# Performance work log

Hardware: AMD Instinct MI355X
Metric: run time of the kernel (lower is better)

The kernel has to match this reference:

```python
import jax, jax.numpy as jnp
import numpy as np

NUM_HEADS = 16


def setup_inputs() -> dict:
    key = jax.random.key(0)
    ks = jax.random.split(key, 7)
    B, S, H = 4, 1024, 1024
    s = 0.02
    return {
        "x": jax.random.normal(ks[0], (B, S, H), dtype=jnp.float32),
        "Wq": jax.random.normal(ks[1], (H, H), dtype=jnp.float32) * s,
        "bq": jax.random.normal(ks[2], (H,), dtype=jnp.float32) * s,
        "Wk": jax.random.normal(ks[3], (H, H), dtype=jnp.float32) * s,
        "bk": jax.random.normal(ks[4], (H,), dtype=jnp.float32) * s,
        "Wv": jax.random.normal(ks[5], (H, H), dtype=jnp.float32) * s,
        "bv": jax.random.normal(ks[6], (H,), dtype=jnp.float32) * s,
    }


def _split_heads(y, num_heads):
    # rearrange 'b s (h c) -> h b s c'
    b, s, hid = y.shape
    c = hid // num_heads
    return y.reshape(b, s, num_heads, c).transpose(2, 0, 1, 3)


def reference(x, Wq, bq, Wk, bk, Wv, bv):
    h = NUM_HEADS
    head_size = x.shape[-1] // h
    # torch Linear: y = x @ W.T + b
    q = _split_heads(x @ Wq.T + bq, h)  # [h,b,s,c]
    k = _split_heads(x @ Wk.T + bk, h)
    v = _split_heads(x @ Wv.T + bv, h)
    scores = jnp.einsum('hbfc,hbtc->hbft', q, k) / jnp.sqrt(
        jnp.asarray(head_size, x.dtype))
    patterns = jax.nn.softmax(scores, axis=-1)  # softmax over t
    # NOTE: faithful to source, contracts over f (query axis) per
    # einsum('hbft,hbfc->hbtc', patterns, value)
    av = jnp.einsum('hbft,hbfc->hbtc', patterns, v)  # [h,b,t,c]
    # rearrange 'h b s c -> b s (c h)'  (channel-major interleave)
    out = av.transpose(1, 2, 3, 0)  # [b,s,c,h]
    b, s, c, hh = out.shape
    return out.reshape(b, s, c * hh)
```

## Files before the change

kernel.cpp:

```cpp
#include <hip/hip_runtime.h>
#include <hip/hip_bf16.h>

typedef short bf16x8 __attribute__((ext_vector_type(8)));
typedef short bf16x4 __attribute__((ext_vector_type(4)));
typedef float f32x4 __attribute__((ext_vector_type(4)));
typedef unsigned short u16;

#define MFMA32(a, b, c) __builtin_amdgcn_mfma_f32_16x16x32_bf16(a, b, c, 0, 0, 0)

#if defined(__has_builtin)
#if __has_builtin(__builtin_amdgcn_mfma_f32_16x16x16bf16_1k)
#define HAVE_MFMA16 1
#define MFMA16(a, b, c) __builtin_amdgcn_mfma_f32_16x16x16bf16_1k(a, b, c, 0, 0, 0)
#endif
#endif
#ifndef HAVE_MFMA16
static __device__ inline f32x4 mfma16_asm(bf16x4 a, bf16x4 b, f32x4 c) {
    f32x4 d;
    asm volatile("v_mfma_f32_16x16x16_bf16 %0, %1, %2, %3\n\ts_nop 7\n\ts_nop 7"
                 : "=v"(d) : "v"(a), "v"(b), "v"(c));
    return d;
}
#define MFMA16(a, b, c) mfma16_asm(a, b, c)
#endif

__device__ inline float fexp2(float x) {
#if defined(__has_builtin) && __has_builtin(__builtin_amdgcn_exp2f)
    return __builtin_amdgcn_exp2f(x);
#else
    return exp2f(x);
#endif
}

__device__ inline u16 f2bf(float f) {
    unsigned u = __float_as_uint(f);
    unsigned r = (u + 0x7fffu + ((u >> 16) & 1u)) >> 16;
    return (u16)r;
}

__device__ inline float bf2f(u16 v) {
    return __uint_as_float(((unsigned)v) << 16);
}

__device__ inline void gload_lds16(const void* g, void* l) {
    __builtin_amdgcn_global_load_lds(
        (const __attribute__((address_space(1))) void*)g,
        (__attribute__((address_space(3))) void*)l, 16, 0, 0);
}

#define BARRIER() __builtin_amdgcn_s_barrier()

__device__ inline int swz(int row, int colbyte) {
    return row * 128 + (colbyte ^ ((row & 7) << 4));
}

__device__ inline void stage8k_512(const u16* __restrict__ g, int gstride,
                                   u16* lds, int tid) {
    int o = tid * 16;
    int row = o >> 7;
    int colb = (o & 127) ^ ((row & 7) << 4);
    gload_lds16(g + row * gstride + (colb >> 1), (char*)lds + o);
}

__device__ inline void stage16k_256(const u16* __restrict__ g, int gstride,
                                    u16* lds, int tid) {
#pragma unroll
    for (int j = 0; j < 4; j++) {
        int o = (tid + j * 256) * 16;
        int row = o >> 7;
        int colb = (o & 127) ^ ((row & 7) << 4);
        gload_lds16(g + row * gstride + (colb >> 1), (char*)lds + o);
    }
}

__global__ void k_convert(const float* __restrict__ src, u16* __restrict__ dst, int n) {
    int i = (blockIdx.x * blockDim.x + threadIdx.x) * 4;
    if (i < n) {
        float4 v = *reinterpret_cast<const float4*>(src + i);
        ushort4 o;
        o.x = f2bf(v.x); o.y = f2bf(v.y); o.z = f2bf(v.z); o.w = f2bf(v.w);
        *reinterpret_cast<ushort4*>(dst + i) = o;
    }
}

__global__ void k_convert3(const float* __restrict__ s0, const float* __restrict__ s1,
                           const float* __restrict__ s2, u16* __restrict__ dst) {
    const float* s = (blockIdx.y == 0) ? s0 : ((blockIdx.y == 1) ? s1 : s2);
    int i = (blockIdx.x * blockDim.x + threadIdx.x) * 4;
    float4 v = *reinterpret_cast<const float4*>(s + i);
    ushort4 o;
    o.x = f2bf(v.x); o.y = f2bf(v.y); o.z = f2bf(v.z); o.w = f2bf(v.w);
    *reinterpret_cast<ushort4*>(dst + blockIdx.y * 1048576 + i) = o;
}

__global__ __launch_bounds__(256, 3) void k_proj(
    const u16* __restrict__ xb, const u16* __restrict__ wb,
    const float* __restrict__ bq, const float* __restrict__ bk, const float* __restrict__ bv,
    u16* __restrict__ outQ, u16* __restrict__ outK, u16* __restrict__ outVt)
{
    __shared__ __align__(16) u16 As[8192];
    __shared__ __align__(16) u16 Bs[8192];
    const int tid = threadIdx.x;
    const int lane = tid & 63;
    const int w = tid >> 6;
    const int bid = blockIdx.x;
    const int xcd = bid & 7, idx = bid >> 3;
    const int mg = xcd & 3, ng = xcd >> 2;
    const int m0 = (mg * 8 + (idx & 7)) * 128;
    const int nfull = ng * 12 + (idx >> 3);
    const int widx = nfull >> 3;
    const int n0 = (nfull & 7) * 128;
    const u16* W = wb + widx * 1024 * 1024;
    const float* bias = (widx == 0) ? bq : ((widx == 1) ? bk : bv);

    const int wm = (w >> 1) * 64, wn = (w & 1) * 64;
    const int lm = lane & 15, lg = lane >> 4;

    f32x4 zero = {0.f, 0.f, 0.f, 0.f};
    f32x4 acc[4][4];
#pragma unroll
    for (int m = 0; m < 4; m++)
#pragma unroll
        for (int n = 0; n < 4; n++) acc[m][n] = zero;

    for (int it = 0; it < 16; ++it) {
        stage16k_256(xb + m0 * 1024 + it * 64, 1024, As, tid);
        stage16k_256(W + n0 * 1024 + it * 64, 1024, Bs, tid);
        __syncthreads();
        const char* Ab = (const char*)As;
        const char* Bb = (const char*)Bs;
#pragma unroll
        for (int kk = 0; kk < 2; kk++) {
            bf16x8 a[4], b[4];
#pragma unroll
            for (int m = 0; m < 4; m++)
                a[m] = *(const bf16x8*)(Ab + swz(wm + m * 16 + lm, kk * 64 + lg * 16));
#pragma unroll
            for (int n = 0; n < 4; n++)
                b[n] = *(const bf16x8*)(Bb + swz(wn + n * 16 + lm, kk * 64 + lg * 16));
#pragma unroll
            for (int m = 0; m < 4; m++)
#pragma unroll
                for (int n = 0; n < 4; n++)
                    acc[m][n] = MFMA32(a[m], b[n], acc[m][n]);
        }
        __syncthreads();
    }

#pragma unroll
    for (int n = 0; n < 4; n++) {
        int col = n0 + wn + n * 16 + lm;
        float bz = bias[col];
        int h = col >> 6, c = col & 63;
#pragma unroll
        for (int m = 0; m < 4; m++) {
#pragma unroll
            for (int r = 0; r < 4; r++) {
                int row = m0 + wm + m * 16 + lg * 4 + r;
                float v = acc[m][n][r] + bz;
                int bb = row >> 10, s = row & 1023;
                int hb = h * 4 + bb;
                if (widx == 0) {
                    outQ[(hb * 1024 + s) * 64 + c] = f2bf(v * 0.18033688011112042f);
                } else if (widx == 1) {
                    outK[(hb * 1024 + s) * 64 + c] = f2bf(v);
                } else {
                    outVt[(hb * 64 + c) * 1024 + s] = f2bf(v);
                }
            }
        }
    }
}

__global__ __launch_bounds__(512, 2) void k_stats(
    const u16* __restrict__ Q, const u16* __restrict__ K, u16* __restrict__ Vt)
{
    __shared__ __align__(16) u16 sK[2][4096];
    __shared__ float linv_lds[256];
    const int bid = blockIdx.x;
    const int hb = (bid & 7) * 8 + ((bid >> 3) & 7);
    const int fb = (bid >> 6) * 256;
    const int tid = threadIdx.x, lane = tid & 63, w = tid >> 6;
    const int lm = lane & 15, lg = lane >> 4;
    const u16* Qh = Q + hb * 65536;
    const u16* Kh = K + hb * 65536;
    u16* Vh = Vt + hb * 65536;

    bf16x8 a[2][2];
#pragma unroll
    for (int fg = 0; fg < 2; fg++) {
        const u16* qp = &Qh[(fb + w * 32 + fg * 16 + lm) * 64 + lg * 8];
        a[fg][0] = *(const bf16x8*)qp;
        a[fg][1] = *(const bf16x8*)(qp + 32);
    }

    float lrun[2][4] = {{0.f, 0.f, 0.f, 0.f}, {0.f, 0.f, 0.f, 0.f}};

    stage8k_512(Kh, 64, sK[0], tid);
    int cur = 0;
    for (int it = 0; it < 16; ++it) {
        if (it < 15) {
            stage8k_512(Kh + (it + 1) * 64 * 64, 64, sK[cur ^ 1], tid);
            asm volatile("s_waitcnt vmcnt(1)" ::: "memory");
        } else {
            asm volatile("s_waitcnt vmcnt(0)" ::: "memory");
        }
        BARRIER();
        const char* base = (const char*)sK[cur];
#pragma unroll
        for (int n = 0; n < 4; n++) {
            int r = n * 16 + lm;
            bf16x8 b0 = *(const bf16x8*)(base + swz(r, lg * 16));
            bf16x8 b1 = *(const bf16x8*)(base + swz(r, 64 + lg * 16));
#pragma unroll
            for (int fg = 0; fg < 2; fg++) {
                f32x4 z = {0.f, 0.f, 0.f, 0.f};
                z = MFMA32(a[fg][0], b0, z);
                z = MFMA32(a[fg][1], b1, z);
                lrun[fg][0] += fexp2(z[0]);
                lrun[fg][1] += fexp2(z[1]);
                lrun[fg][2] += fexp2(z[2]);
                lrun[fg][3] += fexp2(z[3]);
            }
        }
        BARRIER();
        cur ^= 1;
    }
#pragma unroll
    for (int fg = 0; fg < 2; fg++) {
#pragma unroll
        for (int r = 0; r < 4; r++) {
            float s = lrun[fg][r];
            s += __shfl_xor(s, 1);
            s += __shfl_xor(s, 2);
            s += __shfl_xor(s, 4);
            s += __shfl_xor(s, 8);
            if (lm == 0) linv_lds[w * 32 + fg * 16 + lg * 4 + r] = 1.0f / s;
        }
    }
    __syncthreads();
    {
        int c = tid >> 3, f8 = tid & 7;
#pragma unroll
        for (int j = 0; j < 4; j++) {
            int fl = f8 * 8 + j * 64;
            u16* vp = &Vh[c * 1024 + fb + fl];
            union { bf16x8 v; u16 e[8]; } uu, oo;
            uu.v = *(const bf16x8*)vp;
#pragma unroll
            for (int i = 0; i < 8; i++)
                oo.e[i] = f2bf(bf2f(uu.e[i]) * linv_lds[fl + i]);
            *(bf16x8*)vp = oo.v;
        }
    }
}

__global__ __launch_bounds__(512, 2) void k_av(
    const u16* __restrict__ Q, const u16* __restrict__ K, const u16* __restrict__ Vt,
    float* __restrict__ out)
{
    __shared__ __align__(16) u16 sQ[2][4096];
    __shared__ __align__(16) u16 sV[2][4096];
    const int bid = blockIdx.x;
    const int hb = (bid & 7) * 8 + ((bid >> 3) & 7);
    const int tb = (bid >> 6) * 256;
    const int tid = threadIdx.x, lane = tid & 63, w = tid >> 6;
    const int lm = lane & 15, lg = lane >> 4;
    const u16* Qh = Q + hb * 65536;
    const u16* Kh = K + hb * 65536;
    const u16* Vh = Vt + hb * 65536;

    bf16x8 bK[2][2];
#pragma unroll
    for (int tg = 0; tg < 2; tg++) {
        const u16* kp = &Kh[(tb + w * 32 + tg * 16 + lm) * 64 + lg * 8];
        bK[tg][0] = *(const bf16x8*)kp;
        bK[tg][1] = *(const bf16x8*)(kp + 32);
    }

    f32x4 zero = {0.f, 0.f, 0.f, 0.f};
    f32x4 accv[2][4];
#pragma unroll
    for (int tg = 0; tg < 2; tg++)
#pragma unroll
        for (int m = 0; m < 4; m++) accv[tg][m] = zero;

    stage8k_512(Qh, 64, sQ[0], tid);
    stage8k_512(Vh, 1024, sV[0], tid);

    int cur = 0;
    for (int it = 0; it < 16; ++it) {
        if (it < 15) {
            int fn = (it + 1) * 64;
            stage8k_512(Qh + fn * 64, 64, sQ[cur ^ 1], tid);
            stage8k_512(Vh + fn, 1024, sV[cur ^ 1], tid);
            asm volatile("s_waitcnt vmcnt(2)" ::: "memory");
        } else {
            asm volatile("s_waitcnt vmcnt(0)" ::: "memory");
        }
        BARRIER();
        const char* Qb = (const char*)sQ[cur];
        const char* Vb = (const char*)sV[cur];

        bf16x4 bv[4][4];
#pragma unroll
        for (int m = 0; m < 4; m++)
#pragma unroll
            for (int kc = 0; kc < 4; kc++)
                bv[m][kc] = *(const bf16x4*)(Vb + swz(m * 16 + lm, kc * 32 + lg * 8));

        bf16x4 afrag[2][4];
#pragma unroll
        for (int mq = 0; mq < 4; mq++) {
            bf16x8 aq0 = *(const bf16x8*)(Qb + swz(mq * 16 + lm, lg * 16));
            bf16x8 aq1 = *(const bf16x8*)(Qb + swz(mq * 16 + lm, 64 + lg * 16));
#pragma unroll
            for (int tg = 0; tg < 2; tg++) {
                f32x4 z = {0.f, 0.f, 0.f, 0.f};
                z = MFMA32(aq0, bK[tg][0], z);
                z = MFMA32(aq1, bK[tg][1], z);
                union { __hip_bfloat162 h2[2]; bf16x4 v4; } u;
                u.h2[0] = __float22bfloat162_rn(make_float2(fexp2(z[0]), fexp2(z[1])));
                u.h2[1] = __float22bfloat162_rn(make_float2(fexp2(z[2]), fexp2(z[3])));
                afrag[tg][mq] = u.v4;
            }
        }
#pragma unroll
        for (int tg = 0; tg < 2; tg++)
#pragma unroll
            for (int m = 0; m < 4; m++)
#pragma unroll
                for (int kc = 0; kc < 4; kc++)
                    accv[tg][m] = MFMA16(afrag[tg][kc], bv[m][kc], accv[tg][m]);
        BARRIER();
        cur ^= 1;
    }

    const int h = hb >> 2, bb = hb & 3;
#pragma unroll
    for (int tg = 0; tg < 2; tg++) {
#pragma unroll
        for (int m = 0; m < 4; m++) {
#pragma unroll
            for (int r = 0; r < 4; r++) {
                int t = tb + w * 32 + tg * 16 + lg * 4 + r;
                int c = m * 16 + lm;
                out[(bb * 1024 + t) * 1024 + c * 16 + h] = accv[tg][m][r];
            }
        }
    }
}

extern "C" void kernel_launch(void* const* d_in, const int* in_sizes, int n_in,
                              void* d_out, int out_size, void* d_ws, size_t ws_size,
                              hipStream_t stream) {
    const float* x  = (const float*)d_in[0];
    const float* Wq = (const float*)d_in[1];
    const float* bq = (const float*)d_in[2];
    const float* Wk = (const float*)d_in[3];
    const float* bk = (const float*)d_in[4];
    const float* Wv = (const float*)d_in[5];
    const float* bv = (const float*)d_in[6];
    float* out = (float*)d_out;
    char* ws = (char*)d_ws;

    u16* xb = (u16*)ws;
    u16* wb = (u16*)(ws + (8u << 20));
    u16* Qb = (u16*)(ws + (14u << 20));
    u16* Kb = (u16*)(ws + (22u << 20));
    u16* Vt = (u16*)(ws + (30u << 20));

    k_convert<<<4096, 256, 0, stream>>>(x, xb, 4096 * 1024);
    k_convert3<<<dim3(1024, 3), 256, 0, stream>>>(Wq, Wk, Wv, wb);
    k_proj<<<768, 256, 0, stream>>>(xb, wb, bq, bk, bv, Qb, Kb, Vt);
    k_stats<<<256, 512, 0, stream>>>(Qb, Kb, Vt);
    k_av<<<256, 512, 0, stream>>>(Qb, Kb, Vt, out);
}
```

Baseline: 117.8 us.

## Halve per-block tile to 512 blocks and add coalesced interleave output kernel

The stats and AV kernels now cover 128 rows per block instead of 256, which doubles the grid to 512 blocks and raises the occupancy hint to 4 blocks per CU. This spreads the attention work over more CUs. The AV kernel no longer does strided 4-byte scatter stores into the channel-major interleaved output. It writes bf16 results contiguously to a scratch buffer, and a new k_interleave kernel gathers across heads and writes float4 rows. The trade-offs are an extra launch, an extra bf16 rounding of the AV result, and K/V/Q tiles being reloaded by twice as many blocks.

New measurement: 170.1 us. 1.44x slower.

```diff
diff --git a/kernel.cpp b/kernel.cpp
--- a/kernel.cpp
+++ b/kernel.cpp
@@ -172,29 +172,25 @@
     }
 }
 
-__global__ __launch_bounds__(512, 2) void k_stats(
+__global__ __launch_bounds__(512, 4) void k_stats(
     const u16* __restrict__ Q, const u16* __restrict__ K, u16* __restrict__ Vt)
 {
     __shared__ __align__(16) u16 sK[2][4096];
-    __shared__ float linv_lds[256];
+    __shared__ float linv_lds[128];
     const int bid = blockIdx.x;
-    const int hb = (bid & 7) * 8 + ((bid >> 3) & 7);
-    const int fb = (bid >> 6) * 256;
+    const int hb = (bid & 7) * 8 + (bid >> 6);
+    const int fb = ((bid >> 3) & 7) * 128;
     const int tid = threadIdx.x, lane = tid & 63, w = tid >> 6;
     const int lm = lane & 15, lg = lane >> 4;
     const u16* Qh = Q + hb * 65536;
     const u16* Kh = K + hb * 65536;
     u16* Vh = Vt + hb * 65536;
 
-    bf16x8 a[2][2];
-#pragma unroll
-    for (int fg = 0; fg < 2; fg++) {
-        const u16* qp = &Qh[(fb + w * 32 + fg * 16 + lm) * 64 + lg * 8];
-        a[fg][0] = *(const bf16x8*)qp;
-        a[fg][1] = *(const bf16x8*)(qp + 32);
-    }
-
-    float lrun[2][4] = {{0.f, 0.f, 0.f, 0.f}, {0.f, 0.f, 0.f, 0.f}};
+    const u16* qp = &Qh[(fb + w * 16 + lm) * 64 + lg * 8];
+    bf16x8 a0 = *(const bf16x8*)qp;
+    bf16x8 a1 = *(const bf16x8*)(qp + 32);
+
+    float lrun[4] = {0.f, 0.f, 0.f, 0.f};
 
     stage8k_512(Kh, 64, sK[0], tid);
     int cur = 0;
@@ -212,38 +208,32 @@
             int r = n * 16 + lm;
             bf16x8 b0 = *(const bf16x8*)(base + swz(r, lg * 16));
             bf16x8 b1 = *(const bf16x8*)(base + swz(r, 64 + lg * 16));
-#pragma unroll
-            for (int fg = 0; fg < 2; fg++) {
-                f32x4 z = {0.f, 0.f, 0.f, 0.f};
-                z = MFMA32(a[fg][0], b0, z);
-                z = MFMA32(a[fg][1], b1, z);
-                lrun[fg][0] += fexp2(z[0]);
-                lrun[fg][1] += fexp2(z[1]);
-                lrun[fg][2] += fexp2(z[2]);
-                lrun[fg][3] += fexp2(z[3]);
-            }
+            f32x4 z = {0.f, 0.f, 0.f, 0.f};
+            z = MFMA32(a0, b0, z);
+            z = MFMA32(a1, b1, z);
+            lrun[0] += fexp2(z[0]);
+            lrun[1] += fexp2(z[1]);
+            lrun[2] += fexp2(z[2]);
+            lrun[3] += fexp2(z[3]);
         }
         BARRIER();
         cur ^= 1;
     }
 #pragma unroll
-    for (int fg = 0; fg < 2; fg++) {
-#pragma unroll
-        for (int r = 0; r < 4; r++) {
-            float s = lrun[fg][r];
-            s += __shfl_xor(s, 1);
-            s += __shfl_xor(s, 2);
-            s += __shfl_xor(s, 4);
-            s += __shfl_xor(s, 8);
-            if (lm == 0) linv_lds[w * 32 + fg * 16 + lg * 4 + r] = 1.0f / s;
-        }
+    for (int r = 0; r < 4; r++) {
+        float s = lrun[r];
+        s += __shfl_xor(s, 1);
+        s += __shfl_xor(s, 2);
+        s += __shfl_xor(s, 4);
+        s += __shfl_xor(s, 8);
+        if (lm == 0) linv_lds[w * 16 + lg * 4 + r] = 1.0f / s;
     }
     __syncthreads();
     {
         int c = tid >> 3, f8 = tid & 7;
 #pragma unroll
-        for (int j = 0; j < 4; j++) {
-            int fl = f8 * 8 + j * 64;
+        for (int j = 0; j < 2; j++) {
+            int fl = f8 * 16 + j * 8;
             u16* vp = &Vh[c * 1024 + fb + fl];
             union { bf16x8 v; u16 e[8]; } uu, oo;
             uu.v = *(const bf16x8*)vp;
@@ -255,35 +245,29 @@
     }
 }
 
-__global__ __launch_bounds__(512, 2) void k_av(
+__global__ __launch_bounds__(512, 4) void k_av(
     const u16* __restrict__ Q, const u16* __restrict__ K, const u16* __restrict__ Vt,
-    float* __restrict__ out)
+    u16* __restrict__ av_sb)
 {
     __shared__ __align__(16) u16 sQ[2][4096];
     __shared__ __align__(16) u16 sV[2][4096];
     const int bid = blockIdx.x;
-    const int hb = (bid & 7) * 8 + ((bid >> 3) & 7);
-    const int tb = (bid >> 6) * 256;
+    const int hb = (bid & 7) * 8 + (bid >> 6);
+    const int tb = ((bid >> 3) & 7) * 128;
     const int tid = threadIdx.x, lane = tid & 63, w = tid >> 6;
     const int lm = lane & 15, lg = lane >> 4;
     const u16* Qh = Q + hb * 65536;
     const u16* Kh = K + hb * 65536;
     const u16* Vh = Vt + hb * 65536;
 
-    bf16x8 bK[2][2];
-#pragma unroll
-    for (int tg = 0; tg < 2; tg++) {
-        const u16* kp = &Kh[(tb + w * 32 + tg * 16 + lm) * 64 + lg * 8];
-        bK[tg][0] = *(const bf16x8*)kp;
-        bK[tg][1] = *(const bf16x8*)(kp + 32);
-    }
+    const u16* kp = &Kh[(tb + w * 16 + lm) * 64 + lg * 8];
+    bf16x8 bK0 = *(const bf16x8*)kp;
+    bf16x8 bK1 = *(const bf16x8*)(kp + 32);
 
     f32x4 zero = {0.f, 0.f, 0.f, 0.f};
-    f32x4 accv[2][4];
-#pragma unroll
-    for (int tg = 0; tg < 2; tg++)
-#pragma unroll
-        for (int m = 0; m < 4; m++) accv[tg][m] = zero;
+    f32x4 accv[4];
+#pragma unroll
+    for (int m = 0; m < 4; m++) accv[m] = zero;
 
     stage8k_512(Qh, 64, sQ[0], tid);
     stage8k_512(Vh, 1024, sV[0], tid);
@@ -309,45 +293,58 @@
             for (int kc = 0; kc < 4; kc++)
                 bv[m][kc] = *(const bf16x4*)(Vb + swz(m * 16 + lm, kc * 32 + lg * 8));
 
-        bf16x4 afrag[2][4];
+        bf16x4 afrag[4];
 #pragma unroll
         for (int mq = 0; mq < 4; mq++) {
             bf16x8 aq0 = *(const bf16x8*)(Qb + swz(mq * 16 + lm, lg * 16));
             bf16x8 aq1 = *(const bf16x8*)(Qb + swz(mq * 16 + lm, 64 + lg * 16));
-#pragma unroll
-            for (int tg = 0; tg < 2; tg++) {
-                f32x4 z = {0.f, 0.f, 0.f, 0.f};
-                z = MFMA32(aq0, bK[tg][0], z);
-                z = MFMA32(aq1, bK[tg][1], z);
-                union { __hip_bfloat162 h2[2]; bf16x4 v4; } u;
-                u.h2[0] = __float22bfloat162_rn(make_float2(fexp2(z[0]), fexp2(z[1])));
-                u.h2[1] = __float22bfloat162_rn(make_float2(fexp2(z[2]), fexp2(z[3])));
-                afrag[tg][mq] = u.v4;
-            }
-        }
-#pragma unroll
-        for (int tg = 0; tg < 2; tg++)
-#pragma unroll
-            for (int m = 0; m < 4; m++)
-#pragma unroll
-                for (int kc = 0; kc < 4; kc++)
-                    accv[tg][m] = MFMA16(afrag[tg][kc], bv[m][kc], accv[tg][m]);
+            f32x4 z = {0.f, 0.f, 0.f, 0.f};
+            z = MFMA32(aq0, bK0, z);
+            z = MFMA32(aq1, bK1, z);
+            union { __hip_bfloat162 h2[2]; bf16x4 v4; } u;
+            u.h2[0] = __float22bfloat162_rn(make_float2(fexp2(z[0]), fexp2(z[1])));
+            u.h2[1] = __float22bfloat162_rn(make_float2(fexp2(z[2]), fexp2(z[3])));
+            afrag[mq] = u.v4;
+        }
+#pragma unroll
+        for (int m = 0; m < 4; m++)
+#pragma unroll
+            for (int kc = 0; kc < 4; kc++)
+                accv[m] = MFMA16(afrag[kc], bv[m][kc], accv[m]);
         BARRIER();
         cur ^= 1;
     }
 
-    const int h = hb >> 2, bb = hb & 3;
-#pragma unroll
-    for (int tg = 0; tg < 2; tg++) {
-#pragma unroll
-        for (int m = 0; m < 4; m++) {
-#pragma unroll
-            for (int r = 0; r < 4; r++) {
-                int t = tb + w * 32 + tg * 16 + lg * 4 + r;
-                int c = m * 16 + lm;
-                out[(bb * 1024 + t) * 1024 + c * 16 + h] = accv[tg][m][r];
+#pragma unroll
+    for (int m = 0; m < 4; m++) {
+#pragma unroll
+        for (int r = 0; r < 4; r++) {
+            int t = tb + w * 16 + lg * 4 + r;
+            av_sb[hb * 65536 + t * 64 + m * 16 + lm] = f2bf(accv[m][r]);
+        }
+    }
+}
+
+__global__ __launch_bounds__(256) void k_interleave(
+    const u16* __restrict__ av_sb, float* __restrict__ out)
+{
+    const int bid = blockIdx.x;
+    const int bb = bid >> 7, ts = (bid & 127) * 8;
+    const int c = threadIdx.x & 63, tl = threadIdx.x >> 6;
+#pragma unroll
+    for (int p = 0; p < 2; p++) {
+        int t = ts + p * 4 + tl;
+        float4 w[4];
+#pragma unroll
+        for (int q = 0; q < 4; q++) {
+#pragma unroll
+            for (int j = 0; j < 4; j++) {
+                int h = q * 4 + j;
+                ((float*)&w[q])[j] = bf2f(av_sb[((h * 4 + bb) * 1024 + t) * 64 + c]);
             }
         }
+        float4* dst = (float4*)&out[(bb * 1024 + t) * 1024 + c * 16];
+        dst[0] = w[0]; dst[1] = w[1]; dst[2] = w[2]; dst[3] = w[3];
     }
 }
 
@@ -369,10 +366,12 @@
     u16* Qb = (u16*)(ws + (14u << 20));
     u16* Kb = (u16*)(ws + (22u << 20));
     u16* Vt = (u16*)(ws + (30u << 20));
+    u16* av_sb = (u16*)ws;
 
     k_convert<<<4096, 256, 0, stream>>>(x, xb, 4096 * 1024);
     k_convert3<<<dim3(1024, 3), 256, 0, stream>>>(Wq, Wk, Wv, wb);
     k_proj<<<768, 256, 0, stream>>>(xb, wb, bq, bk, bv, Qb, Kb, Vt);
-    k_stats<<<256, 512, 0, stream>>>(Qb, Kb, Vt);
-    k_av<<<256, 512, 0, stream>>>(Qb, Kb, Vt, out);
-}
+    k_stats<<<512, 512, 0, stream>>>(Qb, Kb, Vt);
+    k_av<<<512, 512, 0, stream>>>(Qb, Kb, Vt, av_sb);
+    k_interleave<<<512, 256, 0, stream>>>(av_sb, out);
+}
```

## Apply softmax normalization in AV kernel and add coalesced output interleave pass

Applied to the files above, without the earlier changes.

The stats kernel now writes only per-query inverse row sums to workspace instead of rescaling V in place. The AV kernel loads those factors into LDS and multiplies them into the exponentiated probabilities before the PV MFMAs, and V fragments are now loaded inside the MFMA loop to reduce register pressure. The AV result is written as bf16 in a head-major layout, and a new interleave kernel produces the channel-major fp32 output with vector stores, replacing the strided scattered fp32 stores. This adds a kernel launch and an extra round trip through memory, and the bf16 rounding of the output lowers precision.

New measurement: 103.8 us. 1.13x faster.

```diff
diff --git a/kernel.cpp b/kernel.cpp
--- a/kernel.cpp
+++ b/kernel.cpp
@@ -173,10 +173,9 @@
 }
 
 __global__ __launch_bounds__(512, 2) void k_stats(
-    const u16* __restrict__ Q, const u16* __restrict__ K, u16* __restrict__ Vt)
+    const u16* __restrict__ Q, const u16* __restrict__ K, float* __restrict__ linv_out)
 {
     __shared__ __align__(16) u16 sK[2][4096];
-    __shared__ float linv_lds[256];
     const int bid = blockIdx.x;
     const int hb = (bid & 7) * 8 + ((bid >> 3) & 7);
     const int fb = (bid >> 6) * 256;
@@ -184,7 +183,6 @@
     const int lm = lane & 15, lg = lane >> 4;
     const u16* Qh = Q + hb * 65536;
     const u16* Kh = K + hb * 65536;
-    u16* Vh = Vt + hb * 65536;
 
     bf16x8 a[2][2];
 #pragma unroll
@@ -235,32 +233,19 @@
             s += __shfl_xor(s, 2);
             s += __shfl_xor(s, 4);
             s += __shfl_xor(s, 8);
-            if (lm == 0) linv_lds[w * 32 + fg * 16 + lg * 4 + r] = 1.0f / s;
-        }
-    }
-    __syncthreads();
-    {
-        int c = tid >> 3, f8 = tid & 7;
-#pragma unroll
-        for (int j = 0; j < 4; j++) {
-            int fl = f8 * 8 + j * 64;
-            u16* vp = &Vh[c * 1024 + fb + fl];
-            union { bf16x8 v; u16 e[8]; } uu, oo;
-            uu.v = *(const bf16x8*)vp;
-#pragma unroll
-            for (int i = 0; i < 8; i++)
-                oo.e[i] = f2bf(bf2f(uu.e[i]) * linv_lds[fl + i]);
-            *(bf16x8*)vp = oo.v;
+            if (lm == 0)
+                linv_out[hb * 1024 + fb + w * 32 + fg * 16 + lg * 4 + r] = 1.0f / s;
         }
     }
 }
 
 __global__ __launch_bounds__(512, 2) void k_av(
     const u16* __restrict__ Q, const u16* __restrict__ K, const u16* __restrict__ Vt,
-    float* __restrict__ out)
+    const float* __restrict__ linv, u16* __restrict__ av_sb)
 {
     __shared__ __align__(16) u16 sQ[2][4096];
     __shared__ __align__(16) u16 sV[2][4096];
+    __shared__ __align__(16) float linv_lds[1024];
     const int bid = blockIdx.x;
     const int hb = (bid & 7) * 8 + ((bid >> 3) & 7);
     const int tb = (bid >> 6) * 256;
@@ -269,6 +254,7 @@
     const u16* Qh = Q + hb * 65536;
     const u16* Kh = K + hb * 65536;
     const u16* Vh = Vt + hb * 65536;
+    const float* lh = linv + hb * 1024;
 
     bf16x8 bK[2][2];
 #pragma unroll
@@ -287,6 +273,9 @@
 
     stage8k_512(Qh, 64, sQ[0], tid);
     stage8k_512(Vh, 1024, sV[0], tid);
+    *reinterpret_cast<float2*>(&linv_lds[tid * 2]) =
+        *reinterpret_cast<const float2*>(&lh[tid * 2]);
+    __syncthreads();
 
     int cur = 0;
     for (int it = 0; it < 16; ++it) {
@@ -298,45 +287,44 @@
         } else {
             asm volatile("s_waitcnt vmcnt(0)" ::: "memory");
         }
-        BARRIER();
+        if (it > 0) BARRIER();
         const char* Qb = (const char*)sQ[cur];
         const char* Vb = (const char*)sV[cur];
-
-        bf16x4 bv[4][4];
-#pragma unroll
-        for (int m = 0; m < 4; m++)
-#pragma unroll
-            for (int kc = 0; kc < 4; kc++)
-                bv[m][kc] = *(const bf16x4*)(Vb + swz(m * 16 + lm, kc * 32 + lg * 8));
+        const int fc = it * 64;
 
         bf16x4 afrag[2][4];
 #pragma unroll
         for (int mq = 0; mq < 4; mq++) {
             bf16x8 aq0 = *(const bf16x8*)(Qb + swz(mq * 16 + lm, lg * 16));
             bf16x8 aq1 = *(const bf16x8*)(Qb + swz(mq * 16 + lm, 64 + lg * 16));
+            float4 lv = *reinterpret_cast<const float4*>(&linv_lds[fc + mq * 16 + lg * 4]);
 #pragma unroll
             for (int tg = 0; tg < 2; tg++) {
                 f32x4 z = {0.f, 0.f, 0.f, 0.f};
                 z = MFMA32(aq0, bK[tg][0], z);
                 z = MFMA32(aq1, bK[tg][1], z);
                 union { __hip_bfloat162 h2[2]; bf16x4 v4; } u;
-                u.h2[0] = __float22bfloat162_rn(make_float2(fexp2(z[0]), fexp2(z[1])));
-                u.h2[1] = __float22bfloat162_rn(make_float2(fexp2(z[2]), fexp2(z[3])));
+                u.h2[0] = __float22bfloat162_rn(
+                    make_float2(fexp2(z[0]) * lv.x, fexp2(z[1]) * lv.y));
+                u.h2[1] = __float22bfloat162_rn(
+                    make_float2(fexp2(z[2]) * lv.z, fexp2(z[3]) * lv.w));
                 afrag[tg][mq] = u.v4;
             }
         }
 #pragma unroll
-        for (int tg = 0; tg < 2; tg++)
-#pragma unroll
-            for (int m = 0; m < 4; m++)
-#pragma unroll
-                for (int kc = 0; kc < 4; kc++)
-                    accv[tg][m] = MFMA16(afrag[tg][kc], bv[m][kc], accv[tg][m]);
+        for (int m = 0; m < 4; m++) {
+#pragma unroll
+            for (int kc = 0; kc < 4; kc++) {
+                bf16x4 bv = *(const bf16x4*)(Vb + swz(m * 16 + lm, kc * 32 + lg * 8));
+#pragma unroll
+                for (int tg = 0; tg < 2; tg++)
+                    accv[tg][m] = MFMA16(afrag[tg][kc], bv, accv[tg][m]);
+            }
+        }
         BARRIER();
         cur ^= 1;
     }
 
-    const int h = hb >> 2, bb = hb & 3;
 #pragma unroll
     for (int tg = 0; tg < 2; tg++) {
 #pragma unroll
@@ -344,10 +332,32 @@
 #pragma unroll
             for (int r = 0; r < 4; r++) {
                 int t = tb + w * 32 + tg * 16 + lg * 4 + r;
-                int c = m * 16 + lm;
-                out[(bb * 1024 + t) * 1024 + c * 16 + h] = accv[tg][m][r];
-            }
-        }
+                av_sb[hb * 65536 + t * 64 + m * 16 + lm] = f2bf(accv[tg][m][r]);
+            }
+        }
+    }
+}
+
+__global__ __launch_bounds__(256) void k_interleave(
+    const u16* __restrict__ av_sb, float* __restrict__ out)
+{
+    const int bid = blockIdx.x;
+    const int bb = bid >> 7, ts = (bid & 127) * 8;
+    const int c = threadIdx.x & 63, tl = threadIdx.x >> 6;
+#pragma unroll
+    for (int p = 0; p < 2; p++) {
+        int t = ts + p * 4 + tl;
+        float4 w[4];
+#pragma unroll
+        for (int q = 0; q < 4; q++) {
+#pragma unroll
+            for (int j = 0; j < 4; j++) {
+                int h = q * 4 + j;
+                ((float*)&w[q])[j] = bf2f(av_sb[((h * 4 + bb) * 1024 + t) * 64 + c]);
+            }
+        }
+        float4* dst = (float4*)&out[(bb * 1024 + t) * 1024 + c * 16];
+        dst[0] = w[0]; dst[1] = w[1]; dst[2] = w[2]; dst[3] = w[3];
     }
 }
 
@@ -369,10 +379,13 @@
     u16* Qb = (u16*)(ws + (14u << 20));
     u16* Kb = (u16*)(ws + (22u << 20));
     u16* Vt = (u16*)(ws + (30u << 20));
+    float* linv = (float*)(ws + (38u << 20));
+    u16* av_sb = (u16*)ws;
 
     k_convert<<<4096, 256, 0, stream>>>(x, xb, 4096 * 1024);
     k_convert3<<<dim3(1024, 3), 256, 0, stream>>>(Wq, Wk, Wv, wb);
     k_proj<<<768, 256, 0, stream>>>(xb, wb, bq, bk, bv, Qb, Kb, Vt);
-    k_stats<<<256, 512, 0, stream>>>(Qb, Kb, Vt);
-    k_av<<<256, 512, 0, stream>>>(Qb, Kb, Vt, out);
-}
+    k_stats<<<256, 512, 0, stream>>>(Qb, Kb, linv);
+    k_av<<<256, 512, 0, stream>>>(Qb, Kb, Vt, linv, av_sb);
+    k_interleave<<<512, 256, 0, stream>>>(av_sb, out);
+}
```
